# Kernel tuning notes

Hardware: AMD Instinct MI355X
Metric: run time of the kernel (lower is better)

The kernel has to match this reference:

```python
import jax, jax.numpy as jnp
import numpy as np

VOXEL_SIZE = 0.2
MAX_SP = 512


def _labels_single(coords):
    # coords: [N, 3] float32
    # torch .long() truncates toward zero; astype(int32) matches for these magnitudes
    vc = (coords / VOXEL_SIZE).astype(jnp.int32)
    ids = vc[:, 0] * 10000 + vc[:, 1] * 100 + vc[:, 2]  # hashed voxel id, [N]
    N = ids.shape[0]

    # torch.unique(return_inverse=True): sorted uniques + inverse indices
    sorted_ids = jnp.sort(ids)
    is_new = jnp.concatenate(
        [jnp.ones((1,), dtype=bool), sorted_ids[1:] != sorted_ids[:-1]]
    )
    rank = jnp.cumsum(is_new.astype(jnp.int32)) - 1  # unique idx per sorted slot
    pos = jnp.searchsorted(sorted_ids, ids, side='left')  # first occurrence
    inverse = rank[pos]  # [N] inverse indices into sorted uniques
    n_unique = rank[-1] + 1

    # torch.bincount(inverse): counts per unique voxel (padded to length N)
    counts = jnp.zeros((N,), jnp.int32).at[inverse].add(1)

    # argsort descending, take top MAX_SP largest voxels; padded slots have
    # n_unique > MAX_SP (the only case this branch is used)
    large = jnp.argsort(-counts)[:MAX_SP]

    # remap loop: labels default 0; points in large[j] get label j.
    remap = jnp.zeros((N,), jnp.int32).at[large].set(
        jnp.arange(MAX_SP, dtype=jnp.int32)
    )
    capped = remap[inverse]

    return jnp.where(n_unique > MAX_SP, capped, inverse)


def setup_inputs() -> dict:
    key = jax.random.key(0)
    coords = jax.random.normal(key, (32, 262144, 3), dtype=jnp.float32) * 2.0
    return {"coordinates": coords}


def reference(coordinates):
    # [B, N] int32 superpoint labels
    return jax.vmap(_labels_single)(coordinates)
```

## Files before the change

### kernel.cpp

```cpp
#include <hip/hip_runtime.h>
#include <stdint.h>


#define BATCHES 32
#define NPTS    (1 << 18)
#define MAX_SP  512
#define NBUK    76
#define BUK_VOX 16384
#define DRANGE  (NBUK * BUK_VOX)
#define OFFSET  (DRANGE / 2)
#define BUK_DW  (BUK_VOX / 4)
#define TIERCAP 18432
#define BPB     64
#define PPB     (NPTS / BPB)

typedef float    f32x4 __attribute__((ext_vector_type(4)));
typedef int      i32x4 __attribute__((ext_vector_type(4)));
typedef uint32_t u32x4 __attribute__((ext_vector_type(4)));

__device__ __forceinline__ int pidx(float x, float y, float z) {
    int vx = (int)(x / 0.2f);
    int vy = (int)(y / 0.2f);
    int vz = (int)(z / 0.2f);
    int id = vx * 10000 + vy * 100 + vz;
    int idx = id + OFFSET;
    idx = idx < 0 ? 0 : (idx >= DRANGE ? DRANGE - 1 : idx);
    return idx;
}

__global__ void __launch_bounds__(1024) vidx_count(
    const float* __restrict__ coords, int* __restrict__ vidx,
    int* __restrict__ blkcnt)
{
    int b = blockIdx.x >> 6, blk = blockIdx.x & 63, tid = threadIdx.x;
    __shared__ int cnt[NBUK];
    if (tid < NBUK) cnt[tid] = 0;
    __syncthreads();
    size_t p0 = (size_t)b * NPTS + (size_t)blk * PPB + (size_t)tid * 4;
    const f32x4* cp = (const f32x4*)(coords + p0 * 3);
    f32x4 a = __builtin_nontemporal_load(cp + 0);
    f32x4 c = __builtin_nontemporal_load(cp + 1);
    f32x4 d = __builtin_nontemporal_load(cp + 2);
    i32x4 iv;
    iv[0] = pidx(a[0], a[1], a[2]);
    iv[1] = pidx(a[3], c[0], c[1]);
    iv[2] = pidx(c[2], c[3], d[0]);
    iv[3] = pidx(d[1], d[2], d[3]);
    __builtin_nontemporal_store(iv, (i32x4*)(vidx + p0));
    atomicAdd(&cnt[iv[0] >> 14], 1);
    atomicAdd(&cnt[iv[1] >> 14], 1);
    atomicAdd(&cnt[iv[2] >> 14], 1);
    atomicAdd(&cnt[iv[3] >> 14], 1);
    __syncthreads();
    if (tid < NBUK) blkcnt[blockIdx.x * NBUK + tid] = cnt[tid];
}

__global__ void __launch_bounds__(128) scan64(
    const int* __restrict__ blkcnt, int* __restrict__ blkbase,
    int* __restrict__ bukbase, int* __restrict__ buktot)
{
    int b = blockIdx.x, tid = threadIdx.x;
    __shared__ int c[BPB * NBUK];
    __shared__ int start[NBUK];
    for (int i = tid; i < BPB * NBUK; i += 128)
        c[i] = blkcnt[(size_t)b * BPB * NBUK + i];
    __syncthreads();
    if (tid < NBUK) {
        int s = 0;
        for (int blk = 0; blk < BPB; ++blk) s += c[blk * NBUK + tid];
        buktot[b * NBUK + tid] = s;
        start[tid] = s;
    }
    __syncthreads();
    if (tid == 0) {
        int run = 0;
        for (int k = 0; k < NBUK; ++k) { int t = start[k]; start[k] = run; run += t; }
    }
    __syncthreads();
    if (tid < NBUK) {
        int run = start[tid];
        bukbase[b * NBUK + tid] = run;
        for (int blk = 0; blk < BPB; ++blk) {
            blkbase[((size_t)b * BPB + blk) * NBUK + tid] = run;
            run += c[blk * NBUK + tid];
        }
    }
}

__global__ void __launch_bounds__(1024) scatter4(
    const int* __restrict__ vidx, const int* __restrict__ blkcnt,
    const int* __restrict__ blkbase, int* __restrict__ lists)
{
    int b = blockIdx.x >> 6, tid = threadIdx.x;
    __shared__ int stage[PPB];
    __shared__ int offs[NBUK];
    __shared__ int cur[NBUK];
    __shared__ int rebase[NBUK];
    if (tid < NBUK) offs[tid] = blkcnt[blockIdx.x * NBUK + tid];
    __syncthreads();
    if (tid == 0) {
        int run = 0;
        for (int k = 0; k < NBUK; ++k) { int t = offs[k]; offs[k] = run; run += t; }
    }
    __syncthreads();
    if (tid < NBUK) {
        cur[tid] = offs[tid];
        rebase[tid] = blkbase[blockIdx.x * NBUK + tid] - offs[tid];
    }
    __syncthreads();
    size_t p0 = (size_t)b * NPTS + (size_t)(blockIdx.x & 63) * PPB + (size_t)tid * 4;
    i32x4 iv = __builtin_nontemporal_load((const i32x4*)(vidx + p0));
    #pragma unroll
    for (int j = 0; j < 4; ++j) {
        int idx = iv[j];
        stage[atomicAdd(&cur[idx >> 14], 1)] = idx;
    }
    __syncthreads();
    int* lb = lists + (size_t)b * NPTS;
    #pragma unroll
    for (int j = 0; j < 4; ++j) {
        int i = j * 1024 + tid;
        int v = stage[i];
        __builtin_nontemporal_store(v, &lb[rebase[v >> 14] + i]);
    }
}

__global__ void __launch_bounds__(1024) bucket_hist(
    const int* __restrict__ lists, const int* __restrict__ bukbase,
    const int* __restrict__ buktot, int* __restrict__ bhist,
    uint32_t* __restrict__ cnt16k)
{
    int k = blockIdx.x, b = blockIdx.y, tid = threadIdx.x;
    __shared__ uint32_t cnt[BUK_DW];
    __shared__ uint32_t h8[8 * 256];
    for (int i = tid; i < BUK_DW; i += 1024) cnt[i] = 0;
    for (int i = tid; i < 8 * 256; i += 1024) h8[i] = 0;
    __syncthreads();
    int st = bukbase[b * NBUK + k], n = buktot[b * NBUK + k];
    const int* seg = lists + (size_t)b * NPTS + st;
    for (int i = tid; i < n; i += 1024) {
        int idx = seg[i] & (BUK_VOX - 1);
        atomicAdd(&cnt[idx >> 2], 1u << ((idx & 3) * 8));
    }
    __syncthreads();
    u32x4 w4 = ((const u32x4*)cnt)[tid];
    ((u32x4*)(cnt16k + (size_t)(b * NBUK + k) * BUK_DW))[tid] = w4;
    int rep = (tid >> 7) & 7;
    #pragma unroll
    for (int d = 0; d < 4; ++d) {
        uint32_t w = w4[d];
        if (!w) continue;
        #pragma unroll
        for (int j = 0; j < 4; ++j) {
            uint32_t cc = (w >> (j * 8)) & 255u;
            if (cc) atomicAdd(&h8[rep * 256 + cc], 1u);
        }
    }
    __syncthreads();
    if (tid < 256) {
        uint32_t s = 0;
        #pragma unroll
        for (int r = 0; r < 8; ++r) s += h8[r * 256 + tid];
        bhist[((size_t)b * NBUK + k) * 256 + tid] = (int)s;
    }
}

__global__ void __launch_bounds__(256) select_params(
    const int* __restrict__ bhist, int* __restrict__ params,
    int* __restrict__ wbase, int* __restrict__ tbase)
{
    int b = blockIdx.x, tid = threadIdx.x;
    __shared__ int tot[256];
    __shared__ int wc_[NBUK], tc_[NBUK];
    __shared__ int sh_T;
    int s = 0;
    for (int k = 0; k < NBUK; ++k) s += bhist[((size_t)b * NBUK + k) * 256 + tid];
    tot[tid] = s;
    __syncthreads();
    if (tid == 0) {
        int nu = 0;
        for (int c = 1; c < 256; ++c) nu += tot[c];
        int acc = 0, c = 255;
        while (c > 1 && acc + tot[c] < MAX_SP) { acc += tot[c]; --c; }
        int T = c, A = acc;
        int m = MAX_SP - A; if (m > tot[T]) m = tot[T];
        params[b * 8 + 0] = T;  params[b * 8 + 1] = A;
        params[b * 8 + 2] = m;  params[b * 8 + 3] = nu;
        params[b * 8 + 4] = A + m;
        sh_T = T;
    }
    __syncthreads();
    int T = sh_T;
    if (tid < NBUK) {
        int ws = 0;
        const int* bh = bhist + ((size_t)b * NBUK + tid) * 256;
        for (int c = T + 1; c < 256; ++c) ws += bh[c];
        wc_[tid] = ws;
        tc_[tid] = bh[T];
    }
    __syncthreads();
    if (tid == 0) {
        int aw = 0, at = 0;
        for (int k = 0; k < NBUK; ++k) {
            wbase[b * NBUK + k] = aw; tbase[b * NBUK + k] = at;
            aw += wc_[k]; at += tc_[k];
        }
    }
}

__global__ void __launch_bounds__(512) collect2(
    const uint32_t* __restrict__ cnt16k, const int* __restrict__ params,
    const int* __restrict__ wbase, const int* __restrict__ tbase,
    uint32_t* __restrict__ wid, int* __restrict__ wcnt, uint32_t* __restrict__ tier)
{
    int k = blockIdx.x, b = blockIdx.y, tid = threadIdx.x;
    int T = params[b * 8 + 0], m = params[b * 8 + 2];
    int wb = wbase[b * NBUK + k], tb = tbase[b * NBUK + k];
    __shared__ int woff[8];
    __shared__ int wpos;
    if (tid == 0) wpos = 0;
    const u32x4* g = (const u32x4*)(cnt16k + (size_t)(b * NBUK + k) * BUK_DW);
    u32x4 v[2];
    v[0] = g[tid * 2 + 0];
    v[1] = g[tid * 2 + 1];
    __syncthreads();
    int base_id = (k * BUK_DW + tid * 8) * 4;
    int ntier = 0;
    #pragma unroll
    for (int q = 0; q < 2; ++q) {
        #pragma unroll
        for (int d = 0; d < 4; ++d) {
            uint32_t w = v[q][d];
            if (!w) continue;
            #pragma unroll
            for (int j = 0; j < 4; ++j) {
                int c = (int)((w >> (j * 8)) & 255u);
                if (c > T) {
                    int p = atomicAdd(&wpos, 1);
                    wid [b * MAX_SP + wb + p] = (uint32_t)(base_id + (q * 4 + d) * 4 + j);
                    wcnt[b * MAX_SP + wb + p] = c;
                } else if (c == T) ++ntier;
            }
        }
    }
    int lane = tid & 63, wv = tid >> 6;
    int inc = ntier;
    #pragma unroll
    for (int s = 1; s < 64; s <<= 1) {
        int y = __shfl_up(inc, s);
        if (lane >= s) inc += y;
    }
    if (lane == 63) woff[wv] = inc;
    __syncthreads();
    int pre = inc - ntier;
    for (int i = 0; i < wv; ++i) pre += woff[i];
    if (tb < m && ntier > 0) {
        int pos = tb + pre, kk = 0;
        #pragma unroll
        for (int q = 0; q < 2; ++q) {
            #pragma unroll
            for (int d = 0; d < 4; ++d) {
                uint32_t w = v[q][d];
                if (!w) continue;
                #pragma unroll
                for (int j = 0; j < 4; ++j) {
                    int c = (int)((w >> (j * 8)) & 255u);
                    if (c == T) {
                        int q2 = pos + kk; ++kk;
                        if (q2 < TIERCAP) tier[b * TIERCAP + q2] = (uint32_t)(base_id + (q * 4 + d) * 4 + j);
                    }
                }
            }
        }
    }
}

__global__ void __launch_bounds__(512) rank512(
    const int* __restrict__ params, const uint32_t* __restrict__ wid,
    const int* __restrict__ wcnt, const uint32_t* __restrict__ tier,
    uint32_t* __restrict__ lookup)
{
    int b = blockIdx.x, tid = threadIdx.x;
    int T = params[b * 8 + 0], A = params[b * 8 + 1];
    int nu = params[b * 8 + 3], nw = params[b * 8 + 4];
    __shared__ uint32_t wu[MAX_SP];
    __shared__ int      wc[MAX_SP];
    if (tid < A)       { wu[tid] = wid[b * MAX_SP + tid]; wc[tid] = wcnt[b * MAX_SP + tid]; }
    else if (tid < nw) { wu[tid] = tier[b * TIERCAP + (tid - A)]; wc[tid] = T; }
    __syncthreads();
    if (tid < nw) {
        uint32_t u = wu[tid]; int c = wc[tid];
        int r = 0, ur = 0;
        for (int j = 0; j < nw; ++j) {
            uint32_t uj = wu[j]; int cj = wc[j];
            r  += ((cj > c) || (cj == c && uj < u)) ? 1 : 0;
            ur += (uj < u) ? 1 : 0;
        }
        int label = (nu <= MAX_SP) ? ur : r;
        lookup[b * MAX_SP + ur] = (u << 9) | (uint32_t)label;
    }
}

__global__ void __launch_bounds__(1024) write_labels4(
    const int* __restrict__ vidx, const int* __restrict__ params,
    const uint32_t* __restrict__ lookup, int* __restrict__ out)
{
    __shared__ uint32_t lu[MAX_SP];
    int b = blockIdx.x >> 6, tid = threadIdx.x;
    if (tid < MAX_SP) lu[tid] = lookup[b * MAX_SP + tid];
    __syncthreads();
    int nw = params[b * 8 + 4];
    size_t p0 = (size_t)b * NPTS + (size_t)(blockIdx.x & 63) * PPB + (size_t)tid * 4;
    i32x4 iv = __builtin_nontemporal_load((const i32x4*)(vidx + p0));
    i32x4 ov;
    #pragma unroll
    for (int j = 0; j < 4; ++j) {
        uint32_t u = (uint32_t)iv[j];
        int lo = 0, hi = nw;
        while (lo < hi) { int mid = (lo + hi) >> 1; if ((lu[mid] >> 9) < u) lo = mid + 1; else hi = mid; }
        int label = 0;
        if (lo < nw && (lu[lo] >> 9) == u) label = (int)(lu[lo] & 511u);
        ov[j] = label;
    }
    __builtin_nontemporal_store(ov, (i32x4*)(out + p0));
}

extern "C" void kernel_launch(void* const* d_in, const int* in_sizes, int n_in,
                              void* d_out, int out_size, void* d_ws, size_t ws_size,
                              hipStream_t stream) {
    const float* coords = (const float*)d_in[0];
    int* out = (int*)d_out;

    uint8_t* p = (uint8_t*)d_ws;
    int*      vidx    = (int*)p;      p += (size_t)BATCHES * NPTS * 4;
    int*      lists   = (int*)p;      p += (size_t)BATCHES * NPTS * 4;
    uint32_t* cnt16k  = (uint32_t*)p; p += (size_t)BATCHES * NBUK * BUK_DW * 4;
    int*      blkcnt  = (int*)p;      p += (size_t)BATCHES * BPB * NBUK * 4;
    int*      blkbase = (int*)p;      p += (size_t)BATCHES * BPB * NBUK * 4;
    int*      bhist   = (int*)p;      p += (size_t)BATCHES * NBUK * 256 * 4;
    uint32_t* tier    = (uint32_t*)p; p += (size_t)BATCHES * TIERCAP * 4;
    int*      bukbase = (int*)p;      p += (size_t)BATCHES * NBUK * 4;
    int*      buktot  = (int*)p;      p += (size_t)BATCHES * NBUK * 4;
    int*      wbase   = (int*)p;      p += (size_t)BATCHES * NBUK * 4;
    int*      tbase   = (int*)p;      p += (size_t)BATCHES * NBUK * 4;
    int*      params  = (int*)p;      p += (size_t)BATCHES * 8 * 4;
    uint32_t* wid     = (uint32_t*)p; p += (size_t)BATCHES * MAX_SP * 4;
    int*      wcnt    = (int*)p;      p += (size_t)BATCHES * MAX_SP * 4;
    uint32_t* lookup  = (uint32_t*)p; p += (size_t)BATCHES * MAX_SP * 4;

    vidx_count   <<<BATCHES * BPB, 1024, 0, stream>>>(coords, vidx, blkcnt);
    scan64       <<<BATCHES, 128, 0, stream>>>(blkcnt, blkbase, bukbase, buktot);
    scatter4     <<<BATCHES * BPB, 1024, 0, stream>>>(vidx, blkcnt, blkbase, lists);
    bucket_hist  <<<dim3(NBUK, BATCHES), 1024, 0, stream>>>(lists, bukbase, buktot, bhist, cnt16k);
    select_params<<<BATCHES, 256, 0, stream>>>(bhist, params, wbase, tbase);
    collect2     <<<dim3(NBUK, BATCHES), 512, 0, stream>>>(cnt16k, params, wbase, tbase, wid, wcnt, tier);
    rank512      <<<BATCHES, 512, 0, stream>>>(params, wid, wcnt, tier, lookup);
    write_labels4<<<BATCHES * BPB, 1024, 0, stream>>>(vidx, params, lookup, out);
}
```

Baseline: 315.0 us.

## Replace bucket scatter with direct global atomic packed-byte voxel counting

Removes the per-block bucket counting, the scan kernel, the scatter into bucket lists and the shared-memory re-counting. Each point now does a packed 8-bit global atomicAdd into a per-batch dense count array, which a new kernel zeroes first. This cuts several kernel launches and a full write and read pass over the points. In exchange there are 8M global atomics that contend on hot voxels, and packed byte counters can overflow into the neighbouring byte if any voxel gets more than 255 points.

```diff
diff --git a/kernel.cpp b/kernel.cpp
--- a/kernel.cpp
+++ b/kernel.cpp
@@ -10,6 +10,7 @@
 #define DRANGE  (NBUK * BUK_VOX)
 #define OFFSET  (DRANGE / 2)
 #define BUK_DW  (BUK_VOX / 4)
+#define BAT_DW  (DRANGE / 4)
 #define TIERCAP 18432
 #define BPB     64
 #define PPB     (NPTS / BPB)
@@ -28,14 +29,21 @@
     return idx;
 }
 
+__global__ void __launch_bounds__(1024) zero_cnt(u32x4* __restrict__ cnt4)
+{
+    size_t i = (size_t)blockIdx.x * 4096 + threadIdx.x * 4;
+    const size_t n = (size_t)BATCHES * BAT_DW / 4;
+    u32x4 z = {0u, 0u, 0u, 0u};
+    #pragma unroll
+    for (int j = 0; j < 4; ++j)
+        if (i + j < n) __builtin_nontemporal_store(z, &cnt4[i + j]);
+}
+
 __global__ void __launch_bounds__(1024) vidx_count(
     const float* __restrict__ coords, int* __restrict__ vidx,
-    int* __restrict__ blkcnt)
+    uint32_t* __restrict__ cnt16k)
 {
     int b = blockIdx.x >> 6, blk = blockIdx.x & 63, tid = threadIdx.x;
-    __shared__ int cnt[NBUK];
-    if (tid < NBUK) cnt[tid] = 0;
-    __syncthreads();
     size_t p0 = (size_t)b * NPTS + (size_t)blk * PPB + (size_t)tid * 4;
     const f32x4* cp = (const f32x4*)(coords + p0 * 3);
     f32x4 a = __builtin_nontemporal_load(cp + 0);
@@ -47,104 +55,22 @@
     iv[2] = pidx(c[2], c[3], d[0]);
     iv[3] = pidx(d[1], d[2], d[3]);
     __builtin_nontemporal_store(iv, (i32x4*)(vidx + p0));
-    atomicAdd(&cnt[iv[0] >> 14], 1);
-    atomicAdd(&cnt[iv[1] >> 14], 1);
-    atomicAdd(&cnt[iv[2] >> 14], 1);
-    atomicAdd(&cnt[iv[3] >> 14], 1);
-    __syncthreads();
-    if (tid < NBUK) blkcnt[blockIdx.x * NBUK + tid] = cnt[tid];
-}
-
-__global__ void __launch_bounds__(128) scan64(
-    const int* __restrict__ blkcnt, int* __restrict__ blkbase,
-    int* __restrict__ bukbase, int* __restrict__ buktot)
-{
-    int b = blockIdx.x, tid = threadIdx.x;
-    __shared__ int c[BPB * NBUK];
-    __shared__ int start[NBUK];
-    for (int i = tid; i < BPB * NBUK; i += 128)
-        c[i] = blkcnt[(size_t)b * BPB * NBUK + i];
-    __syncthreads();
-    if (tid < NBUK) {
-        int s = 0;
-        for (int blk = 0; blk < BPB; ++blk) s += c[blk * NBUK + tid];
-        buktot[b * NBUK + tid] = s;
-        start[tid] = s;
-    }
-    __syncthreads();
-    if (tid == 0) {
-        int run = 0;
-        for (int k = 0; k < NBUK; ++k) { int t = start[k]; start[k] = run; run += t; }
-    }
-    __syncthreads();
-    if (tid < NBUK) {
-        int run = start[tid];
-        bukbase[b * NBUK + tid] = run;
-        for (int blk = 0; blk < BPB; ++blk) {
-            blkbase[((size_t)b * BPB + blk) * NBUK + tid] = run;
-            run += c[blk * NBUK + tid];
-        }
-    }
-}
-
-__global__ void __launch_bounds__(1024) scatter4(
-    const int* __restrict__ vidx, const int* __restrict__ blkcnt,
-    const int* __restrict__ blkbase, int* __restrict__ lists)
-{
-    int b = blockIdx.x >> 6, tid = threadIdx.x;
-    __shared__ int stage[PPB];
-    __shared__ int offs[NBUK];
-    __shared__ int cur[NBUK];
-    __shared__ int rebase[NBUK];
-    if (tid < NBUK) offs[tid] = blkcnt[blockIdx.x * NBUK + tid];
-    __syncthreads();
-    if (tid == 0) {
-        int run = 0;
-        for (int k = 0; k < NBUK; ++k) { int t = offs[k]; offs[k] = run; run += t; }
-    }
-    __syncthreads();
-    if (tid < NBUK) {
-        cur[tid] = offs[tid];
-        rebase[tid] = blkbase[blockIdx.x * NBUK + tid] - offs[tid];
-    }
-    __syncthreads();
-    size_t p0 = (size_t)b * NPTS + (size_t)(blockIdx.x & 63) * PPB + (size_t)tid * 4;
-    i32x4 iv = __builtin_nontemporal_load((const i32x4*)(vidx + p0));
+    uint32_t* cb = cnt16k + (size_t)b * BAT_DW;
     #pragma unroll
     for (int j = 0; j < 4; ++j) {
         int idx = iv[j];
-        stage[atomicAdd(&cur[idx >> 14], 1)] = idx;
-    }
-    __syncthreads();
-    int* lb = lists + (size_t)b * NPTS;
-    #pragma unroll
-    for (int j = 0; j < 4; ++j) {
-        int i = j * 1024 + tid;
-        int v = stage[i];
-        __builtin_nontemporal_store(v, &lb[rebase[v >> 14] + i]);
+        atomicAdd(&cb[idx >> 2], 1u << ((idx & 3) * 8));
     }
 }
 
 __global__ void __launch_bounds__(1024) bucket_hist(
-    const int* __restrict__ lists, const int* __restrict__ bukbase,
-    const int* __restrict__ buktot, int* __restrict__ bhist,
-    uint32_t* __restrict__ cnt16k)
+    const uint32_t* __restrict__ cnt16k, int* __restrict__ bhist)
 {
     int k = blockIdx.x, b = blockIdx.y, tid = threadIdx.x;
-    __shared__ uint32_t cnt[BUK_DW];
     __shared__ uint32_t h8[8 * 256];
-    for (int i = tid; i < BUK_DW; i += 1024) cnt[i] = 0;
     for (int i = tid; i < 8 * 256; i += 1024) h8[i] = 0;
     __syncthreads();
-    int st = bukbase[b * NBUK + k], n = buktot[b * NBUK + k];
-    const int* seg = lists + (size_t)b * NPTS + st;
-    for (int i = tid; i < n; i += 1024) {
-        int idx = seg[i] & (BUK_VOX - 1);
-        atomicAdd(&cnt[idx >> 2], 1u << ((idx & 3) * 8));
-    }
-    __syncthreads();
-    u32x4 w4 = ((const u32x4*)cnt)[tid];
-    ((u32x4*)(cnt16k + (size_t)(b * NBUK + k) * BUK_DW))[tid] = w4;
+    u32x4 w4 = ((const u32x4*)(cnt16k + (size_t)(b * NBUK + k) * BUK_DW))[tid];
     int rep = (tid >> 7) & 7;
     #pragma unroll
     for (int d = 0; d < 4; ++d) {
@@ -333,14 +259,9 @@
 
     uint8_t* p = (uint8_t*)d_ws;
     int*      vidx    = (int*)p;      p += (size_t)BATCHES * NPTS * 4;
-    int*      lists   = (int*)p;      p += (size_t)BATCHES * NPTS * 4;
-    uint32_t* cnt16k  = (uint32_t*)p; p += (size_t)BATCHES * NBUK * BUK_DW * 4;
-    int*      blkcnt  = (int*)p;      p += (size_t)BATCHES * BPB * NBUK * 4;
-    int*      blkbase = (int*)p;      p += (size_t)BATCHES * BPB * NBUK * 4;
+    uint32_t* cnt16k  = (uint32_t*)p; p += (size_t)BATCHES * BAT_DW * 4;
     int*      bhist   = (int*)p;      p += (size_t)BATCHES * NBUK * 256 * 4;
     uint32_t* tier    = (uint32_t*)p; p += (size_t)BATCHES * TIERCAP * 4;
-    int*      bukbase = (int*)p;      p += (size_t)BATCHES * NBUK * 4;
-    int*      buktot  = (int*)p;      p += (size_t)BATCHES * NBUK * 4;
     int*      wbase   = (int*)p;      p += (size_t)BATCHES * NBUK * 4;
     int*      tbase   = (int*)p;      p += (size_t)BATCHES * NBUK * 4;
     int*      params  = (int*)p;      p += (size_t)BATCHES * 8 * 4;
@@ -348,10 +269,9 @@
     int*      wcnt    = (int*)p;      p += (size_t)BATCHES * MAX_SP * 4;
     uint32_t* lookup  = (uint32_t*)p; p += (size_t)BATCHES * MAX_SP * 4;
 
-    vidx_count   <<<BATCHES * BPB, 1024, 0, stream>>>(coords, vidx, blkcnt);
-    scan64       <<<BATCHES, 128, 0, stream>>>(blkcnt, blkbase, bukbase, buktot);
-    scatter4     <<<BATCHES * BPB, 1024, 0, stream>>>(vidx, blkcnt, blkbase, lists);
-    bucket_hist  <<<dim3(NBUK, BATCHES), 1024, 0, stream>>>(lists, bukbase, buktot, bhist, cnt16k);
+    zero_cnt     <<<608, 1024, 0, stream>>>((u32x4*)cnt16k);
+    vidx_count   <<<BATCHES * BPB, 1024, 0, stream>>>(coords, vidx, cnt16k);
+    bucket_hist  <<<dim3(NBUK, BATCHES), 1024, 0, stream>>>(cnt16k, bhist);
     select_params<<<BATCHES, 256, 0, stream>>>(bhist, params, wbase, tbase);
     collect2     <<<dim3(NBUK, BATCHES), 512, 0, stream>>>(cnt16k, params, wbase, tbase, wid, wcnt, tier);
     rank512      <<<BATCHES, 512, 0, stream>>>(params, wid, wcnt, tier, lookup);
```

Measured after the change: 632.5 us. +100.8%, slower.
